# Optimization experiments

Hardware: AMD Instinct MI355X
Metric: run time of the kernel (lower is better)

## Reference

```python
import jax, jax.numpy as jnp
import numpy as np

B, N, C, G = 32, 1024, 64, 64

def setup_inputs() -> dict:
    key = jax.random.key(0)
    ks = jax.random.split(key, 8)
    return {
        "x": jax.random.normal(ks[0], (B, N, C), dtype=jnp.float32),
        "valid_len": jax.random.randint(ks[1], (B,), 0, N, dtype=jnp.int64) if jax.config.jax_enable_x64 else jax.random.randint(ks[1], (B,), 0, N, dtype=jnp.int32),
        "Wq": jax.random.normal(ks[2], (C, G), dtype=jnp.float32) * 0.1,
        "bq": jax.random.normal(ks[3], (G,), dtype=jnp.float32) * 0.1,
        "Wk": jax.random.normal(ks[4], (C, G), dtype=jnp.float32) * 0.1,
        "bk": jax.random.normal(ks[5], (G,), dtype=jnp.float32) * 0.1,
        "Wv": jax.random.normal(ks[6], (C, G), dtype=jnp.float32) * 0.1,
        "bv": jax.random.normal(ks[7], (G,), dtype=jnp.float32) * 0.1,
    }

def reference(x, valid_len, Wq, bq, Wk, bk, Wv, bv):
    # x: [B, N, C]; valid_len: [B] int (number of valid key positions per batch)
    q = x @ Wq + bq                                   # [B, N, G]
    k = x @ Wk + bk                                   # [B, N, G]
    v = x @ Wv + bv                                   # [B, N, G]
    scores = jnp.einsum('bnd,bmd->bnm', q, k)         # [B, N, N] (no 1/sqrt(d) scale)
    # mask: key positions >= valid_len[b] get -1e6 (matches original's -1000000.0 fill)
    col = jnp.arange(scores.shape[-1])
    mask = col[None, None, :] >= valid_len[:, None, None]
    scores = jnp.where(mask, jnp.float32(-1000000.0), scores)
    attn = jax.nn.softmax(scores, axis=-1)            # [B, N, N]
    return jnp.einsum('bnm,bmd->bnd', attn, v)        # [B, N, G]
```

## Files before the change

kernel.cpp:

```cpp
#include <hip/hip_runtime.h>
#include <stdint.h>


typedef __attribute__((ext_vector_type(4))) float    floatx4;
typedef __attribute__((ext_vector_type(8))) _Float16 halfx8;

static __device__ __forceinline__ unsigned short f2h(float f) {
    union { _Float16 h; unsigned short u; } v; v.h = (_Float16)f;
    return v.u;
}
static __device__ __forceinline__ float h2f(unsigned short u) {
    union { unsigned short u; _Float16 h; } v; v.u = u;
    return (float)v.h;
}

static __device__ __forceinline__ void stage_x(
    unsigned short* xh, unsigned short* xl, const float* __restrict__ x,
    int grow0, int tid)
{
#pragma unroll
    for (int i = 0; i < 2; ++i) {
        int id = i * 256 + tid;
        int r = id >> 3, c8 = id & 7;
        const float4* gp = (const float4*)(x + (grow0 + r) * 64 + c8 * 8);
        float4 f0 = gp[0], f1 = gp[1];
        float fv[8] = { f0.x, f0.y, f0.z, f0.w, f1.x, f1.y, f1.z, f1.w };
        __align__(16) unsigned short thi[8], tlo[8];
#pragma unroll
        for (int j = 0; j < 8; ++j) {
            unsigned short hi = f2h(fv[j]);
            thi[j] = hi;
            tlo[j] = f2h(fv[j] - h2f(hi));
        }
        int idx = r * 64 + ((c8 ^ (r & 7)) * 8);
        *(uint4*)&xh[idx] = *(uint4*)thi;
        *(uint4*)&xl[idx] = *(uint4*)tlo;
    }
}

static __device__ __forceinline__ void stage_w(
    const float* __restrict__ W, unsigned short* hiDst, unsigned short* loDst,
    int tid)
{
    int g = tid & 63, ci = tid >> 6;
#pragma unroll
    for (int j = 0; j < 16; ++j) {
        int c = ci * 16 + j;
        float f = W[c * 64 + g];
        unsigned short hi = f2h(f);
        unsigned short lo = f2h(f - h2f(hi));
        int idx = g * 64 + (((c >> 3) ^ (g & 7)) * 8) + (c & 7);
        hiDst[idx] = hi;
        loDst[idx] = lo;
    }
}

static __device__ __forceinline__ void proj16(
    halfx8 ah0, halfx8 ah1, halfx8 al0, halfx8 al1,
    const unsigned short* bh, const unsigned short* bl,
    const float* __restrict__ bias, int l15, int quad, floatx4* accOut)
{
#pragma unroll
    for (int gs = 0; gs < 4; ++gs) {
        int brow = gs * 16 + l15;
        float bb = bias[gs * 16 + l15];
        floatx4 acc = { bb, bb, bb, bb };
        int bidx0 = brow * 64 + (((0 + quad) ^ (brow & 7)) * 8);
        int bidx1 = brow * 64 + (((4 + quad) ^ (brow & 7)) * 8);
        halfx8 b_hi0 = *(const halfx8*)&bh[bidx0];
        halfx8 b_hi1 = *(const halfx8*)&bh[bidx1];
        halfx8 b_lo0 = *(const halfx8*)&bl[bidx0];
        halfx8 b_lo1 = *(const halfx8*)&bl[bidx1];
        acc = __builtin_amdgcn_mfma_f32_16x16x32_f16(ah0, b_hi0, acc, 0, 0, 0);
        acc = __builtin_amdgcn_mfma_f32_16x16x32_f16(ah1, b_hi1, acc, 0, 0, 0);
        acc = __builtin_amdgcn_mfma_f32_16x16x32_f16(ah0, b_lo0, acc, 0, 0, 0);
        acc = __builtin_amdgcn_mfma_f32_16x16x32_f16(ah1, b_lo1, acc, 0, 0, 0);
        acc = __builtin_amdgcn_mfma_f32_16x16x32_f16(al0, b_hi0, acc, 0, 0, 0);
        acc = __builtin_amdgcn_mfma_f32_16x16x32_f16(al1, b_hi1, acc, 0, 0, 0);
        accOut[gs] = acc;
    }
}

__global__ __launch_bounds__(256, 2) void fused_attn_kernel(
    const float* __restrict__ x,
    const float* __restrict__ Wq, const float* __restrict__ bq,
    const float* __restrict__ Wk, const float* __restrict__ bk,
    const float* __restrict__ Wv, const float* __restrict__ bv,
    const int* __restrict__ valid_len, float* __restrict__ out)
{
    __shared__ __align__(16) unsigned short smem[8 * 4096];

    unsigned short* Q   = &smem[0];
    unsigned short* VS  = &smem[4096];
    unsigned short* XH  = &smem[8192];
    unsigned short* XL  = &smem[12288];
    unsigned short* WK0 = &smem[16384];
    unsigned short* WK1 = &smem[20480];
    unsigned short* WV0 = &smem[24576];
    unsigned short* WV1 = &smem[28672];
    unsigned short* PS  = XH;
    unsigned short* KL  = XL;

    const int tid  = threadIdx.x;
    const int blk  = blockIdx.x;
    const int row0 = blk * 64;
    const int b    = blk >> 4;
    const int lane = tid & 63;
    const int w    = tid >> 6;
    const int l15  = lane & 15;
    const int quad = lane >> 4;
    const int arow = w * 16 + l15;
    const int aidx0 = arow * 64 + (((0 + quad) ^ (arow & 7)) * 8);
    const int aidx1 = arow * 64 + (((4 + quad) ^ (arow & 7)) * 8);

    const int vl    = valid_len[b];
    const int nt    = (vl == 0) ? 16 : ((vl + 63) >> 6);
    const int fullt = vl >> 6;

    stage_x(XH, XL, x, row0, tid);
    stage_w(Wq, VS, WK0, tid);
    __syncthreads();

    {
        halfx8 ah0 = *(const halfx8*)&XH[aidx0];
        halfx8 ah1 = *(const halfx8*)&XH[aidx1];
        halfx8 al0 = *(const halfx8*)&XL[aidx0];
        halfx8 al1 = *(const halfx8*)&XL[aidx1];
        floatx4 qacc[4];
        proj16(ah0, ah1, al0, al1, VS, WK0, bq, l15, quad, qacc);
#pragma unroll
        for (int gs = 0; gs < 4; ++gs) {
            int c8 = gs * 2 + (l15 >> 3);
#pragma unroll
            for (int r = 0; r < 4; ++r) {
                int row = w * 16 + quad * 4 + r;
                Q[row * 64 + ((c8 ^ (row & 7)) * 8) + (l15 & 7)] = f2h(qacc[r][gs == 0 ? 0 : 0] * 0.f + qacc[gs][r]);
            }
        }
    }
    __syncthreads();

    stage_w(Wk, WK0, WK1, tid);
    stage_w(Wv, WV0, WV1, tid);

    halfx8 aq0 = *(const halfx8*)&Q[aidx0];
    halfx8 aq1 = *(const halfx8*)&Q[aidx1];

    float m_r[4]    = { -INFINITY, -INFINITY, -INFINITY, -INFINITY };
    float l_lane[4] = { 0.f, 0.f, 0.f, 0.f };
    floatx4 o[4] = { {0,0,0,0}, {0,0,0,0}, {0,0,0,0}, {0,0,0,0} };

    for (int t = 0; t < nt; ++t) {
        __syncthreads();
        stage_x(XH, XL, x, b * 1024 + t * 64, tid);
        __syncthreads();

        halfx8 kxh0 = *(const halfx8*)&XH[aidx0];
        halfx8 kxh1 = *(const halfx8*)&XH[aidx1];
        halfx8 kxl0 = *(const halfx8*)&XL[aidx0];
        halfx8 kxl1 = *(const halfx8*)&XL[aidx1];
        __syncthreads();

        {
            floatx4 kacc[4], vacc2[4];
            proj16(kxh0, kxh1, kxl0, kxl1, WK0, WK1, bk, l15, quad, kacc);
            proj16(kxh0, kxh1, kxl0, kxl1, WV0, WV1, bv, l15, quad, vacc2);
#pragma unroll
            for (int gs = 0; gs < 4; ++gs) {
                int c8 = gs * 2 + (l15 >> 3);
                int g  = gs * 16 + l15;
#pragma unroll
                for (int r = 0; r < 4; ++r) {
                    int key = w * 16 + quad * 4 + r;
                    KL[key * 64 + ((c8 ^ (key & 7)) * 8) + (l15 & 7)] = f2h(kacc[gs][r]);
                    VS[g * 64 + (((key >> 3) ^ (g & 7)) * 8) + (key & 7)] = f2h(vacc2[gs][r]);
                }
            }
        }
        __syncthreads();

        floatx4 s[4];
#pragma unroll
        for (int sub = 0; sub < 4; ++sub) {
            int krow = sub * 16 + l15;
            halfx8 bk0 = *(const halfx8*)&KL[krow * 64 + (((0 + quad) ^ (krow & 7)) * 8)];
            halfx8 bk1 = *(const halfx8*)&KL[krow * 64 + (((4 + quad) ^ (krow & 7)) * 8)];
            floatx4 acc = { 0, 0, 0, 0 };
            acc = __builtin_amdgcn_mfma_f32_16x16x32_f16(aq0, bk0, acc, 0, 0, 0);
            acc = __builtin_amdgcn_mfma_f32_16x16x32_f16(aq1, bk1, acc, 0, 0, 0);
            s[sub] = acc;
        }
        if (t >= fullt) {
#pragma unroll
            for (int sub = 0; sub < 4; ++sub) {
                int key = t * 64 + sub * 16 + l15;
                if (key >= vl) { s[sub][0] = -1e6f; s[sub][1] = -1e6f; s[sub][2] = -1e6f; s[sub][3] = -1e6f; }
            }
        }

        float p[4][4];
        float alpha[4];
#pragma unroll
        for (int r = 0; r < 4; ++r) {
            float mx = fmaxf(fmaxf(s[0][r], s[1][r]), fmaxf(s[2][r], s[3][r]));
#pragma unroll
            for (int off = 1; off < 16; off <<= 1)
                mx = fmaxf(mx, __shfl_xor(mx, off, 64));
            float mnew = fmaxf(m_r[r], mx);
            alpha[r] = __expf(m_r[r] - mnew);
            float psum = 0.f;
#pragma unroll
            for (int sub = 0; sub < 4; ++sub) {
                float pv = __expf(s[sub][r] - mnew);
                p[sub][r] = pv;
                psum += pv;
            }
            l_lane[r] = l_lane[r] * alpha[r] + psum;
            m_r[r] = mnew;
        }
#pragma unroll
        for (int gs = 0; gs < 4; ++gs) {
            o[gs][0] *= alpha[0]; o[gs][1] *= alpha[1];
            o[gs][2] *= alpha[2]; o[gs][3] *= alpha[3];
        }

        unsigned short* psw = &PS[w * 1024];
#pragma unroll
        for (int sub = 0; sub < 4; ++sub) {
            int c8 = sub * 2 + (l15 >> 3);
#pragma unroll
            for (int r = 0; r < 4; ++r) {
                int row = quad * 4 + r;
                psw[row * 64 + ((c8 ^ (row & 7)) * 8) + (l15 & 7)] = f2h(p[sub][r]);
            }
        }
        halfx8 ap0 = *(const halfx8*)&psw[l15 * 64 + (((0 + quad) ^ (l15 & 7)) * 8)];
        halfx8 ap1 = *(const halfx8*)&psw[l15 * 64 + (((4 + quad) ^ (l15 & 7)) * 8)];

#pragma unroll
        for (int gs = 0; gs < 4; ++gs) {
            int grow = gs * 16 + l15;
            halfx8 bv0 = *(const halfx8*)&VS[grow * 64 + (((0 + quad) ^ (grow & 7)) * 8)];
            halfx8 bv1 = *(const halfx8*)&VS[grow * 64 + (((4 + quad) ^ (grow & 7)) * 8)];
            o[gs] = __builtin_amdgcn_mfma_f32_16x16x32_f16(ap0, bv0, o[gs], 0, 0, 0);
            o[gs] = __builtin_amdgcn_mfma_f32_16x16x32_f16(ap1, bv1, o[gs], 0, 0, 0);
        }
    }

    float l[4];
#pragma unroll
    for (int r = 0; r < 4; ++r) {
        float ss = l_lane[r];
#pragma unroll
        for (int off = 1; off < 16; off <<= 1)
            ss += __shfl_xor(ss, off, 64);
        l[r] = ss;
    }
#pragma unroll
    for (int gs = 0; gs < 4; ++gs) {
#pragma unroll
        for (int r = 0; r < 4; ++r) {
            int row = row0 + w * 16 + quad * 4 + r;
            out[row * 64 + gs * 16 + l15] = o[gs][r] / l[r];
        }
    }
}

extern "C" void kernel_launch(void* const* d_in, const int* in_sizes, int n_in,
                              void* d_out, int out_size, void* d_ws, size_t ws_size,
                              hipStream_t stream) {
    const float* x    = (const float*)d_in[0];
    const int*   vlen = (const int*)  d_in[1];
    const float* Wq   = (const float*)d_in[2];
    const float* bq   = (const float*)d_in[3];
    const float* Wk   = (const float*)d_in[4];
    const float* bk   = (const float*)d_in[5];
    const float* Wv   = (const float*)d_in[6];
    const float* bv   = (const float*)d_in[7];
    float* out = (float*)d_out;

    fused_attn_kernel<<<512, 256, 0, stream>>>(
        x, Wq, bq, Wk, bk, Wv, bv, vlen, out);
}
```

Baseline: 114.9 us.

## Drop split-precision K/V projection and double-buffer x tiles with register prefetch

The K and V projections now use only the fp16 high part of x and the weights (2 MFMAs per output tile instead of 6), and the low-part weight buffers are removed. The x tile for the next key block is prefetched into registers before the barrier and written into a second LDS buffer, so one barrier pair per iteration is eliminated and global loads overlap compute. The Q projection keeps the hi/lo split. Keys and values lose the extra fp16 residual precision, which may increase error against the fp32 reference.

```diff
diff --git a/kernel.cpp b/kernel.cpp
--- a/kernel.cpp
+++ b/kernel.cpp
@@ -14,9 +14,34 @@
     return (float)v.h;
 }
 
-static __device__ __forceinline__ void stage_x(
-    unsigned short* xh, unsigned short* xl, const float* __restrict__ x,
-    int grow0, int tid)
+static __device__ __forceinline__ void stage_w_split(
+    const float* __restrict__ W, unsigned short* hiDst, unsigned short* loDst,
+    int tid)
+{
+    int g = tid & 63, ci = tid >> 6;
+#pragma unroll
+    for (int j = 0; j < 16; ++j) {
+        int c = ci * 16 + j;
+        float f = W[c * 64 + g];
+        unsigned short hi = f2h(f);
+        int idx = g * 64 + (((c >> 3) ^ (g & 7)) * 8) + (c & 7);
+        hiDst[idx] = hi;
+        loDst[idx] = f2h(f - h2f(hi));
+    }
+}
+static __device__ __forceinline__ void stage_w_hi(
+    const float* __restrict__ W, unsigned short* hiDst, int tid)
+{
+    int g = tid & 63, ci = tid >> 6;
+#pragma unroll
+    for (int j = 0; j < 16; ++j) {
+        int c = ci * 16 + j;
+        int idx = g * 64 + (((c >> 3) ^ (g & 7)) * 8) + (c & 7);
+        hiDst[idx] = f2h(W[c * 64 + g]);
+    }
+}
+static __device__ __forceinline__ void stage_x_hi(
+    unsigned short* xh, const float* __restrict__ x, int grow0, int tid)
 {
 #pragma unroll
     for (int i = 0; i < 2; ++i) {
@@ -25,59 +50,10 @@
         const float4* gp = (const float4*)(x + (grow0 + r) * 64 + c8 * 8);
         float4 f0 = gp[0], f1 = gp[1];
         float fv[8] = { f0.x, f0.y, f0.z, f0.w, f1.x, f1.y, f1.z, f1.w };
-        __align__(16) unsigned short thi[8], tlo[8];
-#pragma unroll
-        for (int j = 0; j < 8; ++j) {
-            unsigned short hi = f2h(fv[j]);
-            thi[j] = hi;
-            tlo[j] = f2h(fv[j] - h2f(hi));
-        }
-        int idx = r * 64 + ((c8 ^ (r & 7)) * 8);
-        *(uint4*)&xh[idx] = *(uint4*)thi;
-        *(uint4*)&xl[idx] = *(uint4*)tlo;
-    }
-}
-
-static __device__ __forceinline__ void stage_w(
-    const float* __restrict__ W, unsigned short* hiDst, unsigned short* loDst,
-    int tid)
-{
-    int g = tid & 63, ci = tid >> 6;
-#pragma unroll
-    for (int j = 0; j < 16; ++j) {
-        int c = ci * 16 + j;
-        float f = W[c * 64 + g];
-        unsigned short hi = f2h(f);
-        unsigned short lo = f2h(f - h2f(hi));
-        int idx = g * 64 + (((c >> 3) ^ (g & 7)) * 8) + (c & 7);
-        hiDst[idx] = hi;
-        loDst[idx] = lo;
-    }
-}
-
-static __device__ __forceinline__ void proj16(
-    halfx8 ah0, halfx8 ah1, halfx8 al0, halfx8 al1,
-    const unsigned short* bh, const unsigned short* bl,
-    const float* __restrict__ bias, int l15, int quad, floatx4* accOut)
-{
-#pragma unroll
-    for (int gs = 0; gs < 4; ++gs) {
-        int brow = gs * 16 + l15;
-        float bb = bias[gs * 16 + l15];
-        floatx4 acc = { bb, bb, bb, bb };
-        int bidx0 = brow * 64 + (((0 + quad) ^ (brow & 7)) * 8);
-        int bidx1 = brow * 64 + (((4 + quad) ^ (brow & 7)) * 8);
-        halfx8 b_hi0 = *(const halfx8*)&bh[bidx0];
-        halfx8 b_hi1 = *(const halfx8*)&bh[bidx1];
-        halfx8 b_lo0 = *(const halfx8*)&bl[bidx0];
-        halfx8 b_lo1 = *(const halfx8*)&bl[bidx1];
-        acc = __builtin_amdgcn_mfma_f32_16x16x32_f16(ah0, b_hi0, acc, 0, 0, 0);
-        acc = __builtin_amdgcn_mfma_f32_16x16x32_f16(ah1, b_hi1, acc, 0, 0, 0);
-        acc = __builtin_amdgcn_mfma_f32_16x16x32_f16(ah0, b_lo0, acc, 0, 0, 0);
-        acc = __builtin_amdgcn_mfma_f32_16x16x32_f16(ah1, b_lo1, acc, 0, 0, 0);
-        acc = __builtin_amdgcn_mfma_f32_16x16x32_f16(al0, b_hi0, acc, 0, 0, 0);
-        acc = __builtin_amdgcn_mfma_f32_16x16x32_f16(al1, b_hi1, acc, 0, 0, 0);
-        accOut[gs] = acc;
+        __align__(16) unsigned short thi[8];
+#pragma unroll
+        for (int j = 0; j < 8; ++j) thi[j] = f2h(fv[j]);
+        *(uint4*)&xh[r * 64 + ((c8 ^ (r & 7)) * 8)] = *(uint4*)thi;
     }
 }
 
@@ -92,14 +68,12 @@
 
     unsigned short* Q   = &smem[0];
     unsigned short* VS  = &smem[4096];
-    unsigned short* XH  = &smem[8192];
-    unsigned short* XL  = &smem[12288];
-    unsigned short* WK0 = &smem[16384];
-    unsigned short* WK1 = &smem[20480];
-    unsigned short* WV0 = &smem[24576];
-    unsigned short* WV1 = &smem[28672];
-    unsigned short* PS  = XH;
-    unsigned short* KL  = XL;
+    unsigned short* XH0 = &smem[8192];
+    unsigned short* XH1 = &smem[12288];
+    unsigned short* KL  = &smem[16384];
+    unsigned short* PS  = &smem[20480];
+    unsigned short* WK0 = &smem[24576];
+    unsigned short* WV0 = &smem[28672];
 
     const int tid  = threadIdx.x;
     const int blk  = blockIdx.x;
@@ -117,31 +91,62 @@
     const int nt    = (vl == 0) ? 16 : ((vl + 63) >> 6);
     const int fullt = vl >> 6;
 
-    stage_x(XH, XL, x, row0, tid);
-    stage_w(Wq, VS, WK0, tid);
+#pragma unroll
+    for (int i = 0; i < 2; ++i) {
+        int id = i * 256 + tid;
+        int r = id >> 3, c8 = id & 7;
+        const float4* gp = (const float4*)(x + (row0 + r) * 64 + c8 * 8);
+        float4 f0 = gp[0], f1 = gp[1];
+        float fv[8] = { f0.x, f0.y, f0.z, f0.w, f1.x, f1.y, f1.z, f1.w };
+        __align__(16) unsigned short thi[8], tlo[8];
+#pragma unroll
+        for (int j = 0; j < 8; ++j) {
+            unsigned short hi = f2h(fv[j]);
+            thi[j] = hi;
+            tlo[j] = f2h(fv[j] - h2f(hi));
+        }
+        int idx = r * 64 + ((c8 ^ (r & 7)) * 8);
+        *(uint4*)&XH0[idx] = *(uint4*)thi;
+        *(uint4*)&KL[idx]  = *(uint4*)tlo;
+    }
+    stage_w_split(Wq, WK0, PS, tid);
     __syncthreads();
 
     {
-        halfx8 ah0 = *(const halfx8*)&XH[aidx0];
-        halfx8 ah1 = *(const halfx8*)&XH[aidx1];
-        halfx8 al0 = *(const halfx8*)&XL[aidx0];
-        halfx8 al1 = *(const halfx8*)&XL[aidx1];
-        floatx4 qacc[4];
-        proj16(ah0, ah1, al0, al1, VS, WK0, bq, l15, quad, qacc);
+        halfx8 ah0 = *(const halfx8*)&XH0[aidx0];
+        halfx8 ah1 = *(const halfx8*)&XH0[aidx1];
+        halfx8 al0 = *(const halfx8*)&KL[aidx0];
+        halfx8 al1 = *(const halfx8*)&KL[aidx1];
 #pragma unroll
         for (int gs = 0; gs < 4; ++gs) {
+            int brow = gs * 16 + l15;
+            float bb = bq[gs * 16 + l15];
+            floatx4 acc = { bb, bb, bb, bb };
+            int bidx0 = brow * 64 + (((0 + quad) ^ (brow & 7)) * 8);
+            int bidx1 = brow * 64 + (((4 + quad) ^ (brow & 7)) * 8);
+            halfx8 b_hi0 = *(const halfx8*)&WK0[bidx0];
+            halfx8 b_hi1 = *(const halfx8*)&WK0[bidx1];
+            halfx8 b_lo0 = *(const halfx8*)&PS[bidx0];
+            halfx8 b_lo1 = *(const halfx8*)&PS[bidx1];
+            acc = __builtin_amdgcn_mfma_f32_16x16x32_f16(ah0, b_hi0, acc, 0, 0, 0);
+            acc = __builtin_amdgcn_mfma_f32_16x16x32_f16(ah1, b_hi1, acc, 0, 0, 0);
+            acc = __builtin_amdgcn_mfma_f32_16x16x32_f16(ah0, b_lo0, acc, 0, 0, 0);
+            acc = __builtin_amdgcn_mfma_f32_16x16x32_f16(ah1, b_lo1, acc, 0, 0, 0);
+            acc = __builtin_amdgcn_mfma_f32_16x16x32_f16(al0, b_hi0, acc, 0, 0, 0);
+            acc = __builtin_amdgcn_mfma_f32_16x16x32_f16(al1, b_hi1, acc, 0, 0, 0);
             int c8 = gs * 2 + (l15 >> 3);
 #pragma unroll
             for (int r = 0; r < 4; ++r) {
                 int row = w * 16 + quad * 4 + r;
-                Q[row * 64 + ((c8 ^ (row & 7)) * 8) + (l15 & 7)] = f2h(qacc[r][gs == 0 ? 0 : 0] * 0.f + qacc[gs][r]);
+                Q[row * 64 + ((c8 ^ (row & 7)) * 8) + (l15 & 7)] = f2h(acc[r]);
             }
         }
     }
     __syncthreads();
 
-    stage_w(Wk, WK0, WK1, tid);
-    stage_w(Wv, WV0, WV1, tid);
+    stage_w_hi(Wk, WK0, tid);
+    stage_w_hi(Wv, WV0, tid);
+    stage_x_hi(XH0, x, b * 1024 + 0, tid);
 
     halfx8 aq0 = *(const halfx8*)&Q[aidx0];
     halfx8 aq1 = *(const halfx8*)&Q[aidx1];
@@ -150,30 +155,58 @@
     float l_lane[4] = { 0.f, 0.f, 0.f, 0.f };
     floatx4 o[4] = { {0,0,0,0}, {0,0,0,0}, {0,0,0,0}, {0,0,0,0} };
 
+    const int r_a  = tid >> 3,          c8_a = tid & 7;
+    const int r_b  = (256 + tid) >> 3,  c8_b = tid & 7;
+    const int lidx_a = r_a * 64 + ((c8_a ^ (r_a & 7)) * 8);
+    const int lidx_b = r_b * 64 + ((c8_b ^ (r_b & 7)) * 8);
+
     for (int t = 0; t < nt; ++t) {
+        bool pre = (t + 1) < nt;
+        float4 pf[4];
+        if (pre) {
+            const float* xp = x + (b * 1024 + (t + 1) * 64) * 64;
+            pf[0] = ((const float4*)(xp + r_a * 64 + c8_a * 8))[0];
+            pf[1] = ((const float4*)(xp + r_a * 64 + c8_a * 8))[1];
+            pf[2] = ((const float4*)(xp + r_b * 64 + c8_b * 8))[0];
+            pf[3] = ((const float4*)(xp + r_b * 64 + c8_b * 8))[1];
+        }
         __syncthreads();
-        stage_x(XH, XL, x, b * 1024 + t * 64, tid);
-        __syncthreads();
-
-        halfx8 kxh0 = *(const halfx8*)&XH[aidx0];
-        halfx8 kxh1 = *(const halfx8*)&XH[aidx1];
-        halfx8 kxl0 = *(const halfx8*)&XL[aidx0];
-        halfx8 kxl1 = *(const halfx8*)&XL[aidx1];
-        __syncthreads();
+        if (pre) {
+            unsigned short* xn = ((t + 1) & 1) ? XH1 : XH0;
+            __align__(16) unsigned short ta[8] = {
+                f2h(pf[0].x), f2h(pf[0].y), f2h(pf[0].z), f2h(pf[0].w),
+                f2h(pf[1].x), f2h(pf[1].y), f2h(pf[1].z), f2h(pf[1].w) };
+            __align__(16) unsigned short tb[8] = {
+                f2h(pf[2].x), f2h(pf[2].y), f2h(pf[2].z), f2h(pf[2].w),
+                f2h(pf[3].x), f2h(pf[3].y), f2h(pf[3].z), f2h(pf[3].w) };
+            *(uint4*)&xn[lidx_a] = *(uint4*)ta;
+            *(uint4*)&xn[lidx_b] = *(uint4*)tb;
+        }
+        const unsigned short* XHc = (t & 1) ? XH1 : XH0;
+        halfx8 kxh0 = *(const halfx8*)&XHc[aidx0];
+        halfx8 kxh1 = *(const halfx8*)&XHc[aidx1];
 
         {
-            floatx4 kacc[4], vacc2[4];
-            proj16(kxh0, kxh1, kxl0, kxl1, WK0, WK1, bk, l15, quad, kacc);
-            proj16(kxh0, kxh1, kxl0, kxl1, WV0, WV1, bv, l15, quad, vacc2);
 #pragma unroll
             for (int gs = 0; gs < 4; ++gs) {
+                int brow = gs * 16 + l15;
+                int bidx0 = brow * 64 + (((0 + quad) ^ (brow & 7)) * 8);
+                int bidx1 = brow * 64 + (((4 + quad) ^ (brow & 7)) * 8);
+                float bbk = bk[gs * 16 + l15];
+                float bbv = bv[gs * 16 + l15];
+                floatx4 kacc = { bbk, bbk, bbk, bbk };
+                floatx4 vacc = { bbv, bbv, bbv, bbv };
+                kacc = __builtin_amdgcn_mfma_f32_16x16x32_f16(kxh0, *(const halfx8*)&WK0[bidx0], kacc, 0, 0, 0);
+                kacc = __builtin_amdgcn_mfma_f32_16x16x32_f16(kxh1, *(const halfx8*)&WK0[bidx1], kacc, 0, 0, 0);
+                vacc = __builtin_amdgcn_mfma_f32_16x16x32_f16(kxh0, *(const halfx8*)&WV0[bidx0], vacc, 0, 0, 0);
+                vacc = __builtin_amdgcn_mfma_f32_16x16x32_f16(kxh1, *(const halfx8*)&WV0[bidx1], vacc, 0, 0, 0);
                 int c8 = gs * 2 + (l15 >> 3);
                 int g  = gs * 16 + l15;
 #pragma unroll
                 for (int r = 0; r < 4; ++r) {
                     int key = w * 16 + quad * 4 + r;
-                    KL[key * 64 + ((c8 ^ (key & 7)) * 8) + (l15 & 7)] = f2h(kacc[gs][r]);
-                    VS[g * 64 + (((key >> 3) ^ (g & 7)) * 8) + (key & 7)] = f2h(vacc2[gs][r]);
+                    KL[key * 64 + ((c8 ^ (key & 7)) * 8) + (l15 & 7)] = f2h(kacc[r]);
+                    VS[g * 64 + (((key >> 3) ^ (g & 7)) * 8) + (key & 7)] = f2h(vacc[r]);
                 }
             }
         }
```

Result: faster. 105.6 us (-8.1%).

## Double-buffer K/V tiles, prefetch next x tile, drop fp16 split for K/V projection

Applied to the files above, without the earlier changes.

Restructures the main loop so the K/V projection for tile t+1 is computed into alternate shared buffers while tile t is consumed, with the next x tile prefetched into registers before the barrier. This cuts the per-iteration barriers from three to one. The K/V weights are now held in registers and use a single fp16 pass instead of the hi/lo split, which removes four of the six projection MFMAs per group. Each wave stages only its own 16 x rows. The trade-offs are lower accuracy for K and V, higher register pressure, and a smaller shared-memory footprint.

```diff
diff --git a/kernel.cpp b/kernel.cpp
--- a/kernel.cpp
+++ b/kernel.cpp
@@ -14,72 +14,7 @@
     return (float)v.h;
 }
 
-static __device__ __forceinline__ void stage_x(
-    unsigned short* xh, unsigned short* xl, const float* __restrict__ x,
-    int grow0, int tid)
-{
-#pragma unroll
-    for (int i = 0; i < 2; ++i) {
-        int id = i * 256 + tid;
-        int r = id >> 3, c8 = id & 7;
-        const float4* gp = (const float4*)(x + (grow0 + r) * 64 + c8 * 8);
-        float4 f0 = gp[0], f1 = gp[1];
-        float fv[8] = { f0.x, f0.y, f0.z, f0.w, f1.x, f1.y, f1.z, f1.w };
-        __align__(16) unsigned short thi[8], tlo[8];
-#pragma unroll
-        for (int j = 0; j < 8; ++j) {
-            unsigned short hi = f2h(fv[j]);
-            thi[j] = hi;
-            tlo[j] = f2h(fv[j] - h2f(hi));
-        }
-        int idx = r * 64 + ((c8 ^ (r & 7)) * 8);
-        *(uint4*)&xh[idx] = *(uint4*)thi;
-        *(uint4*)&xl[idx] = *(uint4*)tlo;
-    }
-}
-
-static __device__ __forceinline__ void stage_w(
-    const float* __restrict__ W, unsigned short* hiDst, unsigned short* loDst,
-    int tid)
-{
-    int g = tid & 63, ci = tid >> 6;
-#pragma unroll
-    for (int j = 0; j < 16; ++j) {
-        int c = ci * 16 + j;
-        float f = W[c * 64 + g];
-        unsigned short hi = f2h(f);
-        unsigned short lo = f2h(f - h2f(hi));
-        int idx = g * 64 + (((c >> 3) ^ (g & 7)) * 8) + (c & 7);
-        hiDst[idx] = hi;
-        loDst[idx] = lo;
-    }
-}
-
-static __device__ __forceinline__ void proj16(
-    halfx8 ah0, halfx8 ah1, halfx8 al0, halfx8 al1,
-    const unsigned short* bh, const unsigned short* bl,
-    const float* __restrict__ bias, int l15, int quad, floatx4* accOut)
-{
-#pragma unroll
-    for (int gs = 0; gs < 4; ++gs) {
-        int brow = gs * 16 + l15;
-        float bb = bias[gs * 16 + l15];
-        floatx4 acc = { bb, bb, bb, bb };
-        int bidx0 = brow * 64 + (((0 + quad) ^ (brow & 7)) * 8);
-        int bidx1 = brow * 64 + (((4 + quad) ^ (brow & 7)) * 8);
-        halfx8 b_hi0 = *(const halfx8*)&bh[bidx0];
-        halfx8 b_hi1 = *(const halfx8*)&bh[bidx1];
-        halfx8 b_lo0 = *(const halfx8*)&bl[bidx0];
-        halfx8 b_lo1 = *(const halfx8*)&bl[bidx1];
-        acc = __builtin_amdgcn_mfma_f32_16x16x32_f16(ah0, b_hi0, acc, 0, 0, 0);
-        acc = __builtin_amdgcn_mfma_f32_16x16x32_f16(ah1, b_hi1, acc, 0, 0, 0);
-        acc = __builtin_amdgcn_mfma_f32_16x16x32_f16(ah0, b_lo0, acc, 0, 0, 0);
-        acc = __builtin_amdgcn_mfma_f32_16x16x32_f16(ah1, b_lo1, acc, 0, 0, 0);
-        acc = __builtin_amdgcn_mfma_f32_16x16x32_f16(al0, b_hi0, acc, 0, 0, 0);
-        acc = __builtin_amdgcn_mfma_f32_16x16x32_f16(al1, b_hi1, acc, 0, 0, 0);
-        accOut[gs] = acc;
-    }
-}
+#define MFMA16(a, bb, c) __builtin_amdgcn_mfma_f32_16x16x32_f16((a), (bb), (c), 0, 0, 0)
 
 __global__ __launch_bounds__(256, 2) void fused_attn_kernel(
     const float* __restrict__ x,
@@ -88,18 +23,10 @@
     const float* __restrict__ Wv, const float* __restrict__ bv,
     const int* __restrict__ valid_len, float* __restrict__ out)
 {
-    __shared__ __align__(16) unsigned short smem[8 * 4096];
-
-    unsigned short* Q   = &smem[0];
-    unsigned short* VS  = &smem[4096];
-    unsigned short* XH  = &smem[8192];
-    unsigned short* XL  = &smem[12288];
-    unsigned short* WK0 = &smem[16384];
-    unsigned short* WK1 = &smem[20480];
-    unsigned short* WV0 = &smem[24576];
-    unsigned short* WV1 = &smem[28672];
-    unsigned short* PS  = XH;
-    unsigned short* KL  = XL;
+    __shared__ __align__(16) unsigned short smem[28672];
+
+    const int Q_OFF = 0, XH_OFF = 4096, KL0_OFF = 8192, KL1_OFF = 12288,
+              VS0_OFF = 16384, VS1_OFF = 20480, PS_OFF = 24576;
 
     const int tid  = threadIdx.x;
     const int blk  = blockIdx.x;
@@ -109,85 +36,204 @@
     const int w    = tid >> 6;
     const int l15  = lane & 15;
     const int quad = lane >> 4;
-    const int arow = w * 16 + l15;
-    const int aidx0 = arow * 64 + (((0 + quad) ^ (arow & 7)) * 8);
-    const int aidx1 = arow * 64 + (((4 + quad) ^ (arow & 7)) * 8);
+
+    const int xsl  = XH_OFF + w * 1024;
+    const int fidx0 = l15 * 64 + (((0 + quad) ^ (l15 & 7)) * 8);
+    const int fidx1 = l15 * 64 + (((4 + quad) ^ (l15 & 7)) * 8);
+    const int rl   = lane >> 2;
+    const int c8a  = lane & 3;
+    const int c8b  = (lane & 3) + 4;
+    const int sidx_a = rl * 64 + ((c8a ^ (rl & 7)) * 8);
+    const int sidx_b = rl * 64 + ((c8b ^ (rl & 7)) * 8);
 
     const int vl    = valid_len[b];
     const int nt    = (vl == 0) ? 16 : ((vl + 63) >> 6);
     const int fullt = vl >> 6;
 
-    stage_x(XH, XL, x, row0, tid);
-    stage_w(Wq, VS, WK0, tid);
+    {
+        const float* xrow = x + (size_t)(row0 + w * 16) * 64;
+#pragma unroll
+        for (int i = 0; i < 2; ++i) {
+            int c8 = (i == 0) ? c8a : c8b;
+            int sidx = (i == 0) ? sidx_a : sidx_b;
+            const float4* gp = (const float4*)(xrow + rl * 64 + c8 * 8);
+            float4 f0 = gp[0], f1 = gp[1];
+            float fv[8] = { f0.x, f0.y, f0.z, f0.w, f1.x, f1.y, f1.z, f1.w };
+            __align__(16) unsigned short thi[8], tlo[8];
+#pragma unroll
+            for (int j = 0; j < 8; ++j) {
+                unsigned short hi = f2h(fv[j]);
+                thi[j] = hi;
+                tlo[j] = f2h(fv[j] - h2f(hi));
+            }
+            *(uint4*)&smem[xsl + sidx]               = *(uint4*)thi;
+            *(uint4*)&smem[VS0_OFF + w * 1024 + sidx] = *(uint4*)tlo;
+        }
+    }
+    {
+        int g = tid & 63, ci = tid >> 6;
+#pragma unroll
+        for (int j = 0; j < 16; ++j) {
+            int c = ci * 16 + j;
+            int idx = g * 64 + (((c >> 3) ^ (g & 7)) * 8) + (c & 7);
+            float fq = Wq[c * 64 + g];
+            unsigned short qhi = f2h(fq);
+            smem[KL0_OFF + idx] = qhi;
+            smem[KL1_OFF + idx] = f2h(fq - h2f(qhi));
+            smem[VS1_OFF + idx] = f2h(Wk[c * 64 + g]);
+            smem[PS_OFF  + idx] = f2h(Wv[c * 64 + g]);
+        }
+    }
     __syncthreads();
 
-    {
-        halfx8 ah0 = *(const halfx8*)&XH[aidx0];
-        halfx8 ah1 = *(const halfx8*)&XH[aidx1];
-        halfx8 al0 = *(const halfx8*)&XL[aidx0];
-        halfx8 al1 = *(const halfx8*)&XL[aidx1];
-        floatx4 qacc[4];
-        proj16(ah0, ah1, al0, al1, VS, WK0, bq, l15, quad, qacc);
+    halfx8 wkf0[4], wkf1[4], wvf0[4], wvf1[4];
+#pragma unroll
+    for (int gs = 0; gs < 4; ++gs) {
+        int brow = gs * 16 + l15;
+        int b0 = brow * 64 + (((0 + quad) ^ (brow & 7)) * 8);
+        int b1 = brow * 64 + (((4 + quad) ^ (brow & 7)) * 8);
+        wkf0[gs] = *(const halfx8*)&smem[VS1_OFF + b0];
+        wkf1[gs] = *(const halfx8*)&smem[VS1_OFF + b1];
+        wvf0[gs] = *(const halfx8*)&smem[PS_OFF + b0];
+        wvf1[gs] = *(const halfx8*)&smem[PS_OFF + b1];
+    }
+
+    {
+        halfx8 ah0 = *(const halfx8*)&smem[xsl + fidx0];
+        halfx8 ah1 = *(const halfx8*)&smem[xsl + fidx1];
+        halfx8 al0 = *(const halfx8*)&smem[VS0_OFF + w * 1024 + fidx0];
+        halfx8 al1 = *(const halfx8*)&smem[VS0_OFF + w * 1024 + fidx1];
 #pragma unroll
         for (int gs = 0; gs < 4; ++gs) {
+            int brow = gs * 16 + l15;
+            float bb = bq[gs * 16 + l15];
+            floatx4 acc = { bb, bb, bb, bb };
+            int b0 = brow * 64 + (((0 + quad) ^ (brow & 7)) * 8);
+            int b1 = brow * 64 + (((4 + quad) ^ (brow & 7)) * 8);
+            halfx8 bh0 = *(const halfx8*)&smem[KL0_OFF + b0];
+            halfx8 bh1 = *(const halfx8*)&smem[KL0_OFF + b1];
+            halfx8 bl0 = *(const halfx8*)&smem[KL1_OFF + b0];
+            halfx8 bl1 = *(const halfx8*)&smem[KL1_OFF + b1];
+            acc = MFMA16(ah0, bh0, acc);
+            acc = MFMA16(ah1, bh1, acc);
+            acc = MFMA16(ah0, bl0, acc);
+            acc = MFMA16(ah1, bl1, acc);
+            acc = MFMA16(al0, bh0, acc);
+            acc = MFMA16(al1, bh1, acc);
             int c8 = gs * 2 + (l15 >> 3);
 #pragma unroll
             for (int r = 0; r < 4; ++r) {
                 int row = w * 16 + quad * 4 + r;
-                Q[row * 64 + ((c8 ^ (row & 7)) * 8) + (l15 & 7)] = f2h(qacc[r][gs == 0 ? 0 : 0] * 0.f + qacc[gs][r]);
-            }
+                smem[Q_OFF + row * 64 + ((c8 ^ (row & 7)) * 8) + (l15 & 7)] = f2h(acc[r]);
+            }
+        }
+    }
+    const int arow = w * 16 + l15;
+    halfx8 aq0 = *(const halfx8*)&smem[Q_OFF + arow * 64 + (((0 + quad) ^ (arow & 7)) * 8)];
+    halfx8 aq1 = *(const halfx8*)&smem[Q_OFF + arow * 64 + (((4 + quad) ^ (arow & 7)) * 8)];
+
+    {
+        const float* xrow = x + (size_t)(b * 1024 + w * 16) * 64;
+#pragma unroll
+        for (int i = 0; i < 2; ++i) {
+            int c8 = (i == 0) ? c8a : c8b;
+            int sidx = (i == 0) ? sidx_a : sidx_b;
+            const float4* gp = (const float4*)(xrow + rl * 64 + c8 * 8);
+            float4 f0 = gp[0], f1 = gp[1];
+            __align__(16) unsigned short thi[8] = {
+                f2h(f0.x), f2h(f0.y), f2h(f0.z), f2h(f0.w),
+                f2h(f1.x), f2h(f1.y), f2h(f1.z), f2h(f1.w) };
+            *(uint4*)&smem[xsl + sidx] = *(uint4*)thi;
         }
     }
     __syncthreads();
 
-    stage_w(Wk, WK0, WK1, tid);
-    stage_w(Wv, WV0, WV1, tid);
-
-    halfx8 aq0 = *(const halfx8*)&Q[aidx0];
-    halfx8 aq1 = *(const halfx8*)&Q[aidx1];
+    {
+        halfx8 kxh0 = *(const halfx8*)&smem[xsl + fidx0];
+        halfx8 kxh1 = *(const halfx8*)&smem[xsl + fidx1];
+#pragma unroll
+        for (int gs = 0; gs < 4; ++gs) {
+            float bbk = bk[gs * 16 + l15];
+            float bbv = bv[gs * 16 + l15];
+            floatx4 kacc = { bbk, bbk, bbk, bbk };
+            floatx4 vacc = { bbv, bbv, bbv, bbv };
+            kacc = MFMA16(kxh0, wkf0[gs], kacc);
+            kacc = MFMA16(kxh1, wkf1[gs], kacc);
+            vacc = MFMA16(kxh0, wvf0[gs], vacc);
+            vacc = MFMA16(kxh1, wvf1[gs], vacc);
+            int c8 = gs * 2 + (l15 >> 3);
+            int g  = gs * 16 + l15;
+#pragma unroll
+            for (int r = 0; r < 4; ++r) {
+                int key = w * 16 + quad * 4 + r;
+                smem[KL0_OFF + key * 64 + ((c8 ^ (key & 7)) * 8) + (l15 & 7)] = f2h(kacc[r]);
+                smem[VS0_OFF + g * 64 + (((key >> 3) ^ (g & 7)) * 8) + (key & 7)] = f2h(vacc[r]);
+            }
+        }
+    }
 
     float m_r[4]    = { -INFINITY, -INFINITY, -INFINITY, -INFINITY };
     float l_lane[4] = { 0.f, 0.f, 0.f, 0.f };
     floatx4 o[4] = { {0,0,0,0}, {0,0,0,0}, {0,0,0,0}, {0,0,0,0} };
 
     for (int t = 0; t < nt; ++t) {
+        bool pre = (t + 1) < nt;
+        float4 pfa0, pfa1, pfb0, pfb1;
+        if (pre) {
+            const float* xrow = x + (size_t)(b * 1024 + (t + 1) * 64 + w * 16) * 64;
+            pfa0 = ((const float4*)(xrow + rl * 64 + c8a * 8))[0];
+            pfa1 = ((const float4*)(xrow + rl * 64 + c8a * 8))[1];
+            pfb0 = ((const float4*)(xrow + rl * 64 + c8b * 8))[0];
+            pfb1 = ((const float4*)(xrow + rl * 64 + c8b * 8))[1];
+        }
         __syncthreads();
-        stage_x(XH, XL, x, b * 1024 + t * 64, tid);
-        __syncthreads();
-
-        halfx8 kxh0 = *(const halfx8*)&XH[aidx0];
-        halfx8 kxh1 = *(const halfx8*)&XH[aidx1];
-        halfx8 kxl0 = *(const halfx8*)&XL[aidx0];
-        halfx8 kxl1 = *(const halfx8*)&XL[aidx1];
-        __syncthreads();
-
-        {
-            floatx4 kacc[4], vacc2[4];
-            proj16(kxh0, kxh1, kxl0, kxl1, WK0, WK1, bk, l15, quad, kacc);
-            proj16(kxh0, kxh1, kxl0, kxl1, WV0, WV1, bv, l15, quad, vacc2);
+
+        if (pre) {
+            __align__(16) unsigned short ta[8] = {
+                f2h(pfa0.x), f2h(pfa0.y), f2h(pfa0.z), f2h(pfa0.w),
+                f2h(pfa1.x), f2h(pfa1.y), f2h(pfa1.z), f2h(pfa1.w) };
+            __align__(16) unsigned short tb[8] = {
+                f2h(pfb0.x), f2h(pfb0.y), f2h(pfb0.z), f2h(pfb0.w),
+                f2h(pfb1.x), f2h(pfb1.y), f2h(pfb1.z), f2h(pfb1.w) };
+            *(uint4*)&smem[xsl + sidx_a] = *(uint4*)ta;
+            *(uint4*)&smem[xsl + sidx_b] = *(uint4*)tb;
+            halfx8 kxh0 = *(const halfx8*)&smem[xsl + fidx0];
+            halfx8 kxh1 = *(const halfx8*)&smem[xsl + fidx1];
+            const int KLn = ((t + 1) & 1) ? KL1_OFF : KL0_OFF;
+            const int VSn = ((t + 1) & 1) ? VS1_OFF : VS0_OFF;
 #pragma unroll
             for (int gs = 0; gs < 4; ++gs) {
+                float bbk = bk[gs * 16 + l15];
+                float bbv = bv[gs * 16 + l15];
+                floatx4 kacc = { bbk, bbk, bbk, bbk };
+                floatx4 vacc = { bbv, bbv, bbv, bbv };
+                kacc = MFMA16(kxh0, wkf0[gs], kacc);
+                kacc = MFMA16(kxh1, wkf1[gs], kacc);
+                vacc = MFMA16(kxh0, wvf0[gs], vacc);
+                vacc = MFMA16(kxh1, wvf1[gs], vacc);
                 int c8 = gs * 2 + (l15 >> 3);
                 int g  = gs * 16 + l15;
 #pragma unroll
                 for (int r = 0; r < 4; ++r) {
                     int key = w * 16 + quad * 4 + r;
-                    KL[key * 64 + ((c8 ^ (key & 7)) * 8) + (l15 & 7)] = f2h(kacc[gs][r]);
-                    VS[g * 64 + (((key >> 3) ^ (g & 7)) * 8) + (key & 7)] = f2h(vacc2[gs][r]);
+                    smem[KLn + key * 64 + ((c8 ^ (key & 7)) * 8) + (l15 & 7)] = f2h(kacc[r]);
+                    smem[VSn + g * 64 + (((key >> 3) ^ (g & 7)) * 8) + (key & 7)] = f2h(vacc[r]);
                 }
             }
         }
-        __syncthreads();
+
+        const int KLc = (t & 1) ? KL1_OFF : KL0_OFF;
+        const int VSc = (t & 1) ? VS1_OFF : VS0_OFF;
 
         floatx4 s[4];
 #pragma unroll
         for (int sub = 0; sub < 4; ++sub) {
             int krow = sub * 16 + l15;
-            halfx8 bk0 = *(const halfx8*)&KL[krow * 64 + (((0 + quad) ^ (krow & 7)) * 8)];
-            halfx8 bk1 = *(const halfx8*)&KL[krow * 64 + (((4 + quad) ^ (krow & 7)) * 8)];
+            halfx8 bk0 = *(const halfx8*)&smem[KLc + krow * 64 + (((0 + quad) ^ (krow & 7)) * 8)];
+            halfx8 bk1 = *(const halfx8*)&smem[KLc + krow * 64 + (((4 + quad) ^ (krow & 7)) * 8)];
             floatx4 acc = { 0, 0, 0, 0 };
-            acc = __builtin_amdgcn_mfma_f32_16x16x32_f16(aq0, bk0, acc, 0, 0, 0);
-            acc = __builtin_amdgcn_mfma_f32_16x16x32_f16(aq1, bk1, acc, 0, 0, 0);
+            acc = MFMA16(aq0, bk0, acc);
+            acc = MFMA16(aq1, bk1, acc);
             s[sub] = acc;
         }
         if (t >= fullt) {
@@ -224,7 +270,7 @@
             o[gs][2] *= alpha[2]; o[gs][3] *= alpha[3];
         }
 
-        unsigned short* psw = &PS[w * 1024];
+        unsigned short* psw = &smem[PS_OFF + w * 1024];
 #pragma unroll
         for (int sub = 0; sub < 4; ++sub) {
             int c8 = sub * 2 + (l15 >> 3);
@@ -234,16 +280,16 @@
                 psw[row * 64 + ((c8 ^ (row & 7)) * 8) + (l15 & 7)] = f2h(p[sub][r]);
             }
         }
-        halfx8 ap0 = *(const halfx8*)&psw[l15 * 64 + (((0 + quad) ^ (l15 & 7)) * 8)];
-        halfx8 ap1 = *(const halfx8*)&psw[l15 * 64 + (((4 + quad) ^ (l15 & 7)) * 8)];
+        halfx8 ap0 = *(const halfx8*)&psw[fidx0];
+        halfx8 ap1 = *(const halfx8*)&psw[fidx1];
 
 #pragma unroll
         for (int gs = 0; gs < 4; ++gs) {
             int grow = gs * 16 + l15;
-            halfx8 bv0 = *(const halfx8*)&VS[grow * 64 + (((0 + quad) ^ (grow & 7)) * 8)];
-            halfx8 bv1 = *(const halfx8*)&VS[grow * 64 + (((4 + quad) ^ (grow & 7)) * 8)];
-            o[gs] = __builtin_amdgcn_mfma_f32_16x16x32_f16(ap0, bv0, o[gs], 0, 0, 0);
-            o[gs] = __builtin_amdgcn_mfma_f32_16x16x32_f16(ap1, bv1, o[gs], 0, 0, 0);
+            halfx8 bv0 = *(const halfx8*)&smem[VSc + grow * 64 + (((0 + quad) ^ (grow & 7)) * 8)];
+            halfx8 bv1 = *(const halfx8*)&smem[VSc + grow * 64 + (((4 + quad) ^ (grow & 7)) * 8)];
+            o[gs] = MFMA16(ap0, bv0, o[gs]);
+            o[gs] = MFMA16(ap1, bv1, o[gs]);
         }
     }
 
```

Measured after the change: 105.6 us. -8.1%, faster.
